# Optimization experiments

Measured on AMD Instinct MI355X. Metric: run time of the kernel, lower is better.

The kernel has to match this reference:

```python
import jax, jax.numpy as jnp
import numpy as np

N, E, F_IN, D, H = 20000, 640000, 128, 16, 8  # nodes, edges, in_features, out_features, n_heads


def _linear_params(k, fan_in, fan_out):
    W = jax.random.normal(k, (fan_in, fan_out), jnp.float32) / np.sqrt(fan_in)
    b = jnp.zeros((fan_out,), jnp.float32)
    return W, b


def setup_inputs() -> dict:
    key = jax.random.key(0)
    ks = jax.random.split(key, 8)
    x = jax.random.normal(ks[0], (N, F_IN), jnp.float32)
    edge_index = jax.random.randint(ks[1], (2, E), 0, N, dtype=jnp.int64)
    Wq, bq = _linear_params(ks[2], F_IN, D * H)
    Wk, bk = _linear_params(ks[3], F_IN, D * H)
    Wv, bv = _linear_params(ks[4], F_IN, D * H)
    Wpsi, bpsi = _linear_params(ks[5], D, D)
    Wo, bo = _linear_params(ks[6], D * H * 2, F_IN)
    gamma = jnp.ones((F_IN,), jnp.float32)
    beta = jnp.zeros((F_IN,), jnp.float32)
    return {"x": x, "edge_index": edge_index, "Wq": Wq, "bq": bq, "Wk": Wk, "bk": bk,
            "Wv": Wv, "bv": bv, "Wpsi": Wpsi, "bpsi": bpsi, "Wo": Wo, "bo": bo,
            "gamma": gamma, "beta": beta}


def _segment_softmax(logits, seg, num_segments):
    # numerically-stable softmax of edge logits grouped by destination node (row)
    m = jax.ops.segment_max(logits, seg, num_segments=num_segments)  # [N,H]
    m = jnp.where(jnp.isfinite(m), m, 0.0)
    e = jnp.exp(logits - m[seg])  # [E,H]
    s = jax.ops.segment_sum(e, seg, num_segments=num_segments)  # [N,H]
    return e / (s[seg] + 1e-16)


def reference(x, edge_index, Wq, bq, Wk, bk, Wv, bv, Wpsi, bpsi, Wo, bo, gamma, beta):
    q = (x @ Wq + bq).reshape(N, H, D)
    k = (x @ Wk + bk).reshape(N, H, D)
    v = (x @ Wv + bv).reshape(N, H, D)
    row, col = edge_index[0], edge_index[1]

    logits = jnp.einsum('ehd,ehd->eh', q[row], k[col]) / np.sqrt(D)  # [E,H]
    alpha = _segment_softmax(logits, row, N)  # [E,H]

    v_j = v[col]  # [E,H,D]
    h_lp = jax.ops.segment_sum((alpha[..., None] * v_j).reshape(E, H * D), row, num_segments=N)
    v_bp = jnp.tanh(v_j @ Wpsi + bpsi)  # per-head linear on last dim, [E,H,D]
    h_bp = jax.ops.segment_sum((alpha[..., None] * v_bp).reshape(E, H * D), row, num_segments=N)

    h_out = jnp.concatenate([h_lp, h_bp], axis=1) @ Wo + bo  # [N,F_IN]
    y = x + jax.nn.relu(h_out)
    mu = jnp.mean(y, axis=-1, keepdims=True)
    var = jnp.mean(jnp.square(y - mu), axis=-1, keepdims=True)
    return (y - mu) * jax.lax.rsqrt(var + 1e-5) * gamma + beta
```

## Files before the change

kernel.cpp:

```cpp
#include <hip/hip_runtime.h>
#include <hip/hip_bf16.h>
#include <math.h>

#define NN 20000
#define EE 640000

typedef __attribute__((ext_vector_type(8))) short short8;
typedef __attribute__((ext_vector_type(4))) float f32x4;
typedef __hip_bfloat16 bf16;

__device__ inline ushort f2bf(float f) {
  bf16 h = __float2bfloat16(f);
  return *(ushort*)&h;
}
__device__ inline float bflo(uint u) { return __uint_as_float(u << 16); }
__device__ inline float bfhi(uint u) { return __uint_as_float(u & 0xFFFF0000u); }

__global__ __launch_bounds__(256) void prep_scatter(
    const float* __restrict__ x, const int* __restrict__ ei,
    const float* __restrict__ Wq, const float* __restrict__ Wk,
    const float* __restrict__ Wv, const float* __restrict__ Wo,
    const float* __restrict__ Wpsi, const float* __restrict__ bpsi,
    const float* __restrict__ bv,
    ushort* __restrict__ xb, ushort* __restrict__ Wts,
    ushort* __restrict__ Wot, float* __restrict__ bvpsi,
    int* __restrict__ cursor, int* __restrict__ scol) {
  __shared__ float T[128][65];
  __shared__ float WpsiS[256];
  __shared__ float bpsiS[16];
  int b = blockIdx.x, t = threadIdx.x;

  if (b < 2500) {
    int e = b * 256 + t;
    int r = ei[e];
    int c = ei[EE + e];
    int pos = atomicAdd(&cursor[r], 1);
    if (pos < 128) scol[r * 128 + pos] = c;
    return;
  }
  if (b < 3750) {
    int idx = (b - 2500) * 2048 + t * 8;
    float4 f0 = *(const float4*)(x + idx);
    float4 f1 = *(const float4*)(x + idx + 4);
    ushort tmp[8] = {f2bf(f0.x), f2bf(f0.y), f2bf(f0.z), f2bf(f0.w),
                     f2bf(f1.x), f2bf(f1.y), f2bf(f1.z), f2bf(f1.w)};
    *(uint4*)(xb + idx) = *(uint4*)tmp;
    return;
  }
  if (b <= 3754) {
    int which = b - 3750;
    const float* W;
    int k0 = 0, dstride;
    ushort* dst;
    if (which < 3) { W = (which == 0) ? Wq : (which == 1 ? Wk : Wv);
                     dst = Wts + which * 16384; dstride = 128; }
    else { W = Wo; k0 = (which - 3) * 128; dst = Wot; dstride = 256; }
    for (int h2 = 0; h2 < 2; ++h2) {
      int r = t >> 1, c0 = (t & 1) * 32;
      const float* src = W + (size_t)(k0 + r) * 128 + h2 * 64 + c0;
#pragma unroll
      for (int j = 0; j < 8; ++j) {
        float4 f = *(const float4*)(src + 4 * j);
        T[r][c0 + 4 * j + 0] = f.x; T[r][c0 + 4 * j + 1] = f.y;
        T[r][c0 + 4 * j + 2] = f.z; T[r][c0 + 4 * j + 3] = f.w;
      }
      __syncthreads();
      int nl = t >> 2, kc = (t & 3) * 32;
      int n = h2 * 64 + nl;
      ushort buf[32];
#pragma unroll
      for (int k = 0; k < 32; ++k) buf[k] = f2bf(T[kc + k][nl]);
      ushort* dp = dst + (size_t)n * dstride + k0 + kc;
#pragma unroll
      for (int j = 0; j < 4; ++j) *(uint4*)(dp + 8 * j) = ((uint4*)buf)[j];
      __syncthreads();
    }
    return;
  }
  WpsiS[t] = Wpsi[t];
  if (t < 16) bpsiS[t] = bpsi[t];
  for (int h2 = 0; h2 < 2; ++h2) {
    int r = t >> 1, c0 = (t & 1) * 32;
    const float* src = Wv + (size_t)r * 128 + h2 * 64 + c0;
#pragma unroll
    for (int j = 0; j < 8; ++j) {
      float4 f = *(const float4*)(src + 4 * j);
      T[r][c0 + 4 * j + 0] = f.x; T[r][c0 + 4 * j + 1] = f.y;
      T[r][c0 + 4 * j + 2] = f.z; T[r][c0 + 4 * j + 3] = f.w;
    }
    __syncthreads();
    int nl = t >> 2, kc = (t & 3) * 32;
    int n = h2 * 64 + nl;
    int hh = n >> 4, dd = n & 15;
    int lcb = hh * 16 - h2 * 64;
    ushort buf[32];
    for (int k = 0; k < 32; ++k) {
      float acc = 0.f;
#pragma unroll
      for (int dp = 0; dp < 16; ++dp)
        acc = fmaf(T[kc + k][lcb + dp], WpsiS[dp * 16 + dd], acc);
      buf[k] = f2bf(acc);
    }
    ushort* dp2 = Wts + 3 * 16384 + (size_t)n * 128 + kc;
#pragma unroll
    for (int j = 0; j < 4; ++j) *(uint4*)(dp2 + 8 * j) = ((uint4*)buf)[j];
    __syncthreads();
  }
  if (t < 128) {
    int hh = t >> 4, dd = t & 15;
    float acc = bpsiS[dd];
#pragma unroll
    for (int dp = 0; dp < 16; ++dp)
      acc = fmaf(bv[hh * 16 + dp], WpsiS[dp * 16 + dd], acc);
    bvpsi[t] = acc;
  }
}

__global__ __launch_bounds__(256) void qkv_mfma(
    const ushort* __restrict__ xb, const ushort* __restrict__ Wts,
    const float* __restrict__ bq, const float* __restrict__ bk,
    const float* __restrict__ bv, const float* __restrict__ bvpsi,
    ushort* __restrict__ qb, ushort* __restrict__ kvb) {
  __shared__ ushort Tile[128 * 136];
  int t = threadIdx.x;
  int w = t >> 6, lane = t & 63;
  int m = lane & 15, qd = lane >> 4;
  int n0 = blockIdx.x * 128;
  int mat = blockIdx.y;
  const ushort* Wt = Wts + mat * 16384;
  const float* bias = (mat == 0) ? bq : (mat == 1 ? bk : (mat == 2 ? bv : bvpsi));
  int gr0 = n0 + w * 32;

  f32x4 acc0[8], acc1[8];
#pragma unroll
  for (int c = 0; c < 8; ++c) {
    acc0[c] = (f32x4){0.f, 0.f, 0.f, 0.f};
    acc1[c] = (f32x4){0.f, 0.f, 0.f, 0.f};
  }
#pragma unroll
  for (int kb = 0; kb < 4; ++kb) {
    int ko = kb * 32 + qd * 8;
    short8 a0 = *(const short8*)(xb + (size_t)(gr0 + m) * 128 + ko);
    short8 a1 = *(const short8*)(xb + (size_t)(gr0 + 16 + m) * 128 + ko);
#pragma unroll
    for (int c = 0; c < 8; ++c) {
      short8 bfr = *(const short8*)(Wt + (size_t)(c * 16 + m) * 128 + ko);
      acc0[c] = __builtin_amdgcn_mfma_f32_16x16x32_bf16(a0, bfr, acc0[c], 0, 0, 0);
      acc1[c] = __builtin_amdgcn_mfma_f32_16x16x32_bf16(a1, bfr, acc1[c], 0, 0, 0);
    }
  }
#pragma unroll
  for (int c = 0; c < 8; ++c) {
    int col = c * 16 + m;
    float bb = bias[col];
#pragma unroll
    for (int reg = 0; reg < 4; ++reg) {
      float v0 = acc0[c][reg] + bb;
      float v1 = acc1[c][reg] + bb;
      if (mat == 3) { v0 = tanhf(v0); v1 = tanhf(v1); }
      Tile[(w * 32 + 4 * qd + reg) * 136 + col] = f2bf(v0);
      Tile[(w * 32 + 16 + 4 * qd + reg) * 136 + col] = f2bf(v1);
    }
  }
  __syncthreads();
  int row = t >> 1, half = (t & 1) * 64;
  int grow = n0 + row;
  if (grow < NN) {
    const ushort* srcl = &Tile[row * 136 + half];
    ushort* dstg;
    if (mat == 0) dstg = qb + (size_t)grow * 128 + half;
    else dstg = kvb + (size_t)grow * 384 + (mat == 1 ? 0 : (mat == 2 ? 128 : 256)) + half;
#pragma unroll
    for (int j = 0; j < 8; ++j)
      *(uint4*)(dstg + 8 * j) = *(const uint4*)(srcl + 8 * j);
  }
}

__global__ __launch_bounds__(256) void aggregate_kernel(
    const ushort* __restrict__ qb, const ushort* __restrict__ kvb,
    const int* __restrict__ cursor, const int* __restrict__ scol,
    ushort* __restrict__ hb) {
  int wid = threadIdx.x >> 6, lane = threadIdx.x & 63;
  int node = blockIdx.x * 2 + (wid >> 1);
  int e = lane >> 2, h = (wid & 1) * 4 + (lane & 3);
  const float SC = 0.25f * 1.44269504f;

  float qv[16];
  {
    const ushort* qp = qb + (size_t)node * 128 + h * 16;
    uint4 a = *(const uint4*)qp;
    uint4 b = *(const uint4*)(qp + 8);
    uint qq[8] = {a.x, a.y, a.z, a.w, b.x, b.y, b.z, b.w};
#pragma unroll
    for (int i = 0; i < 8; ++i) {
      qv[2 * i] = bflo(qq[i]) * SC;
      qv[2 * i + 1] = bfhi(qq[i]) * SC;
    }
  }
  int cnt = cursor[node];
  cnt = cnt > 128 ? 128 : cnt;
  int base = node * 128;

  float s = 0.f;
  float accV[16], accB[16];
#pragma unroll
  for (int j = 0; j < 16; ++j) { accV[j] = 0.f; accB[j] = 0.f; }

  for (int i0 = 0; i0 < cnt; i0 += 16) {
    int idx = i0 + e;
    bool valid = idx < cnt;
    int col = scol[base + (valid ? idx : 0)];
    const ushort* B = kvb + (size_t)col * 384 + h * 16;
    uint4 ka = *(const uint4*)(B);
    uint4 kb4 = *(const uint4*)(B + 8);
    uint4 va = *(const uint4*)(B + 128);
    uint4 vb4 = *(const uint4*)(B + 136);
    uint4 ta = *(const uint4*)(B + 256);
    uint4 tb4 = *(const uint4*)(B + 264);
    uint kk[8] = {ka.x, ka.y, ka.z, ka.w, kb4.x, kb4.y, kb4.z, kb4.w};
    uint vv[8] = {va.x, va.y, va.z, va.w, vb4.x, vb4.y, vb4.z, vb4.w};
    uint tt[8] = {ta.x, ta.y, ta.z, ta.w, tb4.x, tb4.y, tb4.z, tb4.w};
    float d = 0.f;
#pragma unroll
    for (int i = 0; i < 8; ++i) {
      d = fmaf(qv[2 * i], bflo(kk[i]), d);
      d = fmaf(qv[2 * i + 1], bfhi(kk[i]), d);
    }
    float wgt = valid ? exp2f(d) : 0.f;
    s += wgt;
#pragma unroll
    for (int i = 0; i < 8; ++i) {
      accV[2 * i]     = fmaf(wgt, bflo(vv[i]), accV[2 * i]);
      accV[2 * i + 1] = fmaf(wgt, bfhi(vv[i]), accV[2 * i + 1]);
      accB[2 * i]     = fmaf(wgt, bflo(tt[i]), accB[2 * i]);
      accB[2 * i + 1] = fmaf(wgt, bfhi(tt[i]), accB[2 * i + 1]);
    }
  }

  s += __shfl_xor(s, 32);
#pragma unroll
  for (int j = 0; j < 16; ++j) {
    accV[j] += __shfl_xor(accV[j], 32);
    accB[j] += __shfl_xor(accB[j], 32);
  }
  bool pickV = e < 8;
  float sel[16];
#pragma unroll
  for (int j = 0; j < 16; ++j) sel[j] = pickV ? accV[j] : accB[j];
#pragma unroll
  for (int mask = 4; mask <= 16; mask <<= 1) {
    s += __shfl_xor(s, mask);
#pragma unroll
    for (int j = 0; j < 16; ++j) sel[j] += __shfl_xor(sel[j], mask);
  }
  float inv = s > 0.f ? 1.f / s : 0.f;
  int dg = pickV ? 2 * e : 2 * (e - 8);
  ushort* hp = hb + (size_t)node * 256 + (pickV ? 0 : 128) + h * 16 + dg;
  uint u = (uint)f2bf(sel[dg] * inv) | ((uint)f2bf(sel[dg + 1] * inv) << 16);
  *(uint*)hp = u;
}

__global__ __launch_bounds__(128) void output_mfma(
    const ushort* __restrict__ hb, const ushort* __restrict__ Wot,
    const float* __restrict__ x, const float* __restrict__ bo,
    const float* __restrict__ gamma, const float* __restrict__ beta,
    float* __restrict__ out) {
  int t = threadIdx.x;
  int w = t >> 6, lane = t & 63;
  int m = lane & 15, qd = lane >> 4;
  int gr0 = blockIdx.x * 64 + w * 32;

  f32x4 acc0[8], acc1[8];
#pragma unroll
  for (int c = 0; c < 8; ++c) {
    acc0[c] = (f32x4){0.f, 0.f, 0.f, 0.f};
    acc1[c] = (f32x4){0.f, 0.f, 0.f, 0.f};
  }
#pragma unroll
  for (int kb = 0; kb < 8; ++kb) {
    int ko = kb * 32 + qd * 8;
    short8 a0 = *(const short8*)(hb + (size_t)(gr0 + m) * 256 + ko);
    short8 a1 = *(const short8*)(hb + (size_t)(gr0 + 16 + m) * 256 + ko);
#pragma unroll
    for (int c = 0; c < 8; ++c) {
      short8 bfr = *(const short8*)(Wot + (size_t)(c * 16 + m) * 256 + ko);
      acc0[c] = __builtin_amdgcn_mfma_f32_16x16x32_bf16(a0, bfr, acc0[c], 0, 0, 0);
      acc1[c] = __builtin_amdgcn_mfma_f32_16x16x32_bf16(a1, bfr, acc1[c], 0, 0, 0);
    }
  }
#pragma unroll
  for (int half = 0; half < 2; ++half) {
#pragma unroll
    for (int reg = 0; reg < 4; ++reg) {
      int row = gr0 + half * 16 + 4 * qd + reg;
      bool valid = row < NN;
      float vals[8];
      float sum = 0.f;
#pragma unroll
      for (int c = 0; c < 8; ++c) {
        int col = c * 16 + m;
        float a = (half ? acc1[c][reg] : acc0[c][reg]) + bo[col];
        a = fmaxf(a, 0.f);
        float xv = valid ? x[(size_t)row * 128 + col] : 0.f;
        float v = a + xv;
        vals[c] = v;
        sum += v;
      }
      sum += __shfl_xor(sum, 1); sum += __shfl_xor(sum, 2);
      sum += __shfl_xor(sum, 4); sum += __shfl_xor(sum, 8);
      float mean = sum * (1.f / 128.f);
      float ssq = 0.f;
#pragma unroll
      for (int c = 0; c < 8; ++c) {
        float d = vals[c] - mean;
        ssq = fmaf(d, d, ssq);
      }
      ssq += __shfl_xor(ssq, 1); ssq += __shfl_xor(ssq, 2);
      ssq += __shfl_xor(ssq, 4); ssq += __shfl_xor(ssq, 8);
      float rstd = rsqrtf(ssq * (1.f / 128.f) + 1e-5f);
      if (valid) {
#pragma unroll
        for (int c = 0; c < 8; ++c) {
          int col = c * 16 + m;
          out[(size_t)row * 128 + col] =
              (vals[c] - mean) * rstd * gamma[col] + beta[col];
        }
      }
    }
  }
}

extern "C" void kernel_launch(void* const* d_in, const int* in_sizes, int n_in,
                              void* d_out, int out_size, void* d_ws, size_t ws_size,
                              hipStream_t stream) {
  const float* x     = (const float*)d_in[0];
  const int*   ei    = (const int*)d_in[1];
  const float* Wq    = (const float*)d_in[2];
  const float* bq    = (const float*)d_in[3];
  const float* Wk    = (const float*)d_in[4];
  const float* bk    = (const float*)d_in[5];
  const float* Wv    = (const float*)d_in[6];
  const float* bv    = (const float*)d_in[7];
  const float* Wpsi  = (const float*)d_in[8];
  const float* bpsi  = (const float*)d_in[9];
  const float* Wo    = (const float*)d_in[10];
  const float* bo    = (const float*)d_in[11];
  const float* gamma = (const float*)d_in[12];
  const float* beta  = (const float*)d_in[13];
  float* out = (float*)d_out;

  char* ws = (char*)d_ws;
  ushort* xb    = (ushort*)(ws);
  ushort* qb    = (ushort*)(ws + 5144576);
  ushort* Wts   = (ushort*)(ws + 10289152);
  ushort* Wot   = (ushort*)(ws + 10420224);
  float*  bvpsi = (float*) (ws + 10485760);
  ushort* kvb   = (ushort*)(ws + 10486272);
  ushort* hb    = (ushort*)(ws + 25846272);
  int*    cursor= (int*)   (ws + 36135424);
  int*    scol  = (int*)   (ws + 36215552);

  hipMemsetAsync(cursor, 0, 80000, stream);

  prep_scatter<<<3756, 256, 0, stream>>>(x, ei, Wq, Wk, Wv, Wo, Wpsi, bpsi, bv,
                                         xb, Wts, Wot, bvpsi, cursor, scol);
  qkv_mfma<<<dim3(157, 4), 256, 0, stream>>>(xb, Wts, bq, bk, bv, bvpsi, qb, kvb);
  aggregate_kernel<<<10000, 256, 0, stream>>>(qb, kvb, cursor, scol, hb);
  output_mfma<<<314, 128, 0, stream>>>(hb, Wot, x, bo, gamma, beta, out);
}
```

Before: 247.6 us.

## Pipeline edge gathers in aggregation, stage weights in LDS, coalesce output stores

The aggregation kernel now gives each wave one node, with 8 edges by 8 heads per wave instead of two waves per node. It preloads all neighbour column indices into registers and double-buffers the K/V/psi gathers so the next edge's loads overlap the current edge's arithmetic. Both MFMA GEMM kernels stage their weight matrix in shared memory rather than re-reading it from global memory. The output kernel also writes through an LDS tile to get coalesced float4 stores. These trade more registers and shared memory per block, which can lower occupancy, for better memory-level parallelism and fewer redundant global loads; the output grid also drops from 314 to 313 blocks.

```diff
diff --git a/kernel.cpp b/kernel.cpp
--- a/kernel.cpp
+++ b/kernel.cpp
@@ -121,14 +121,23 @@
     const float* __restrict__ bq, const float* __restrict__ bk,
     const float* __restrict__ bv, const float* __restrict__ bvpsi,
     ushort* __restrict__ qb, ushort* __restrict__ kvb) {
-  __shared__ ushort Tile[128 * 136];
+  __shared__ ushort Bs[128 * 136];
   int t = threadIdx.x;
-  int w = t >> 6, lane = t & 63;
-  int m = lane & 15, qd = lane >> 4;
   int n0 = blockIdx.x * 128;
   int mat = blockIdx.y;
   const ushort* Wt = Wts + mat * 16384;
   const float* bias = (mat == 0) ? bq : (mat == 1 ? bk : (mat == 2 ? bv : bvpsi));
+
+#pragma unroll
+  for (int j = 0; j < 8; ++j) {
+    int idx = j * 256 + t;
+    int row = idx >> 4, ko = (idx & 15) * 8;
+    *(uint4*)&Bs[row * 136 + ko] = *(const uint4*)(Wt + idx * 8);
+  }
+  __syncthreads();
+
+  int w = t >> 6, lane = t & 63;
+  int m = lane & 15, qd = lane >> 4;
   int gr0 = n0 + w * 32;
 
   f32x4 acc0[8], acc1[8];
@@ -144,11 +153,12 @@
     short8 a1 = *(const short8*)(xb + (size_t)(gr0 + 16 + m) * 128 + ko);
 #pragma unroll
     for (int c = 0; c < 8; ++c) {
-      short8 bfr = *(const short8*)(Wt + (size_t)(c * 16 + m) * 128 + ko);
+      short8 bfr = *(const short8*)&Bs[(c * 16 + m) * 136 + ko];
       acc0[c] = __builtin_amdgcn_mfma_f32_16x16x32_bf16(a0, bfr, acc0[c], 0, 0, 0);
       acc1[c] = __builtin_amdgcn_mfma_f32_16x16x32_bf16(a1, bfr, acc1[c], 0, 0, 0);
     }
   }
+  __syncthreads();
 #pragma unroll
   for (int c = 0; c < 8; ++c) {
     int col = c * 16 + m;
@@ -158,18 +168,18 @@
       float v0 = acc0[c][reg] + bb;
       float v1 = acc1[c][reg] + bb;
       if (mat == 3) { v0 = tanhf(v0); v1 = tanhf(v1); }
-      Tile[(w * 32 + 4 * qd + reg) * 136 + col] = f2bf(v0);
-      Tile[(w * 32 + 16 + 4 * qd + reg) * 136 + col] = f2bf(v1);
+      Bs[(w * 32 + 4 * qd + reg) * 136 + col] = f2bf(v0);
+      Bs[(w * 32 + 16 + 4 * qd + reg) * 136 + col] = f2bf(v1);
     }
   }
   __syncthreads();
   int row = t >> 1, half = (t & 1) * 64;
   int grow = n0 + row;
   if (grow < NN) {
-    const ushort* srcl = &Tile[row * 136 + half];
-    ushort* dstg;
-    if (mat == 0) dstg = qb + (size_t)grow * 128 + half;
-    else dstg = kvb + (size_t)grow * 384 + (mat == 1 ? 0 : (mat == 2 ? 128 : 256)) + half;
+    const ushort* srcl = &Bs[row * 136 + half];
+    ushort* dstg = (mat == 0)
+        ? qb + (size_t)grow * 128 + half
+        : kvb + (size_t)grow * 384 + (mat == 1 ? 0 : (mat == 2 ? 128 : 256)) + half;
 #pragma unroll
     for (int j = 0; j < 8; ++j)
       *(uint4*)(dstg + 8 * j) = *(const uint4*)(srcl + 8 * j);
@@ -181,8 +191,8 @@
     const int* __restrict__ cursor, const int* __restrict__ scol,
     ushort* __restrict__ hb) {
   int wid = threadIdx.x >> 6, lane = threadIdx.x & 63;
-  int node = blockIdx.x * 2 + (wid >> 1);
-  int e = lane >> 2, h = (wid & 1) * 4 + (lane & 3);
+  int node = blockIdx.x * 4 + wid;
+  int e = lane >> 3, h = lane & 7;
   const float SC = 0.25f * 1.44269504f;
 
   float qv[16];
@@ -200,33 +210,41 @@
   int cnt = cursor[node];
   cnt = cnt > 128 ? 128 : cnt;
   int base = node * 128;
+  int nv = (cnt + 7) >> 3;
+
+  int cols[16];
+#pragma unroll
+  for (int v = 0; v < 16; ++v) {
+    int idx = v * 8 + e;
+    cols[v] = scol[base + (idx < cnt ? idx : 0)];
+  }
 
   float s = 0.f;
   float accV[16], accB[16];
 #pragma unroll
   for (int j = 0; j < 16; ++j) { accV[j] = 0.f; accB[j] = 0.f; }
 
-  for (int i0 = 0; i0 < cnt; i0 += 16) {
-    int idx = i0 + e;
-    bool valid = idx < cnt;
-    int col = scol[base + (valid ? idx : 0)];
-    const ushort* B = kvb + (size_t)col * 384 + h * 16;
-    uint4 ka = *(const uint4*)(B);
-    uint4 kb4 = *(const uint4*)(B + 8);
-    uint4 va = *(const uint4*)(B + 128);
-    uint4 vb4 = *(const uint4*)(B + 136);
-    uint4 ta = *(const uint4*)(B + 256);
-    uint4 tb4 = *(const uint4*)(B + 264);
-    uint kk[8] = {ka.x, ka.y, ka.z, ka.w, kb4.x, kb4.y, kb4.z, kb4.w};
-    uint vv[8] = {va.x, va.y, va.z, va.w, vb4.x, vb4.y, vb4.z, vb4.w};
-    uint tt[8] = {ta.x, ta.y, ta.z, ta.w, tb4.x, tb4.y, tb4.z, tb4.w};
+  uint4 rA[6], rB[6];
+  auto FETCH = [&](int v, uint4* r) {
+    const ushort* B = kvb + (size_t)cols[v] * 384 + h * 16;
+    r[0] = *(const uint4*)(B);
+    r[1] = *(const uint4*)(B + 8);
+    r[2] = *(const uint4*)(B + 128);
+    r[3] = *(const uint4*)(B + 136);
+    r[4] = *(const uint4*)(B + 256);
+    r[5] = *(const uint4*)(B + 264);
+  };
+  auto CONSUME = [&](int v, const uint4* r) {
+    uint kk[8] = {r[0].x, r[0].y, r[0].z, r[0].w, r[1].x, r[1].y, r[1].z, r[1].w};
+    uint vv[8] = {r[2].x, r[2].y, r[2].z, r[2].w, r[3].x, r[3].y, r[3].z, r[3].w};
+    uint tt[8] = {r[4].x, r[4].y, r[4].z, r[4].w, r[5].x, r[5].y, r[5].z, r[5].w};
     float d = 0.f;
 #pragma unroll
     for (int i = 0; i < 8; ++i) {
       d = fmaf(qv[2 * i], bflo(kk[i]), d);
       d = fmaf(qv[2 * i + 1], bfhi(kk[i]), d);
     }
-    float wgt = valid ? exp2f(d) : 0.f;
+    float wgt = (v * 8 + e < cnt) ? exp2f(d) : 0.f;
     s += wgt;
 #pragma unroll
     for (int i = 0; i < 8; ++i) {
@@ -235,29 +253,35 @@
       accB[2 * i]     = fmaf(wgt, bflo(tt[i]), accB[2 * i]);
       accB[2 * i + 1] = fmaf(wgt, bfhi(tt[i]), accB[2 * i + 1]);
     }
-  }
-
-  s += __shfl_xor(s, 32);
-#pragma unroll
-  for (int j = 0; j < 16; ++j) {
-    accV[j] += __shfl_xor(accV[j], 32);
-    accB[j] += __shfl_xor(accB[j], 32);
-  }
-  bool pickV = e < 8;
-  float sel[16];
-#pragma unroll
-  for (int j = 0; j < 16; ++j) sel[j] = pickV ? accV[j] : accB[j];
-#pragma unroll
-  for (int mask = 4; mask <= 16; mask <<= 1) {
+  };
+
+  if (nv > 0) {
+    FETCH(0, rA);
+    int v = 0;
+    for (; v + 2 <= nv; v += 2) {
+      FETCH(v + 1, rB);
+      CONSUME(v, rA);
+      if (v + 2 < nv) FETCH(v + 2, rA);
+      CONSUME(v + 1, rB);
+    }
+    if (v < nv) CONSUME(v, rA);
+  }
+
+#pragma unroll
+  for (int mask = 8; mask <= 32; mask <<= 1) {
     s += __shfl_xor(s, mask);
 #pragma unroll
-    for (int j = 0; j < 16; ++j) sel[j] += __shfl_xor(sel[j], mask);
+    for (int j = 0; j < 16; ++j) {
+      accV[j] += __shfl_xor(accV[j], mask);
+      accB[j] += __shfl_xor(accB[j], mask);
+    }
   }
   float inv = s > 0.f ? 1.f / s : 0.f;
-  int dg = pickV ? 2 * e : 2 * (e - 8);
-  ushort* hp = hb + (size_t)node * 256 + (pickV ? 0 : 128) + h * 16 + dg;
-  uint u = (uint)f2bf(sel[dg] * inv) | ((uint)f2bf(sel[dg + 1] * inv) << 16);
-  *(uint*)hp = u;
+  int dg = 2 * e;
+  ushort* hp = hb + (size_t)node * 256 + h * 16 + dg;
+  *(uint*)hp = (uint)f2bf(accV[dg] * inv) | ((uint)f2bf(accV[dg + 1] * inv) << 16);
+  *(uint*)(hp + 128) =
+      (uint)f2bf(accB[dg] * inv) | ((uint)f2bf(accB[dg + 1] * inv) << 16);
 }
 
 __global__ __launch_bounds__(128) void output_mfma(
@@ -265,7 +289,16 @@
     const float* __restrict__ x, const float* __restrict__ bo,
     const float* __restrict__ gamma, const float* __restrict__ beta,
     float* __restrict__ out) {
+  __shared__ ushort Bs[128 * 264];
   int t = threadIdx.x;
+#pragma unroll
+  for (int j = 0; j < 32; ++j) {
+    int idx = j * 128 + t;
+    int row = idx >> 5, ko = (idx & 31) * 8;
+    *(uint4*)&Bs[row * 264 + ko] = *(const uint4*)(Wot + idx * 8);
+  }
+  __syncthreads();
+
   int w = t >> 6, lane = t & 63;
   int m = lane & 15, qd = lane >> 4;
   int gr0 = blockIdx.x * 64 + w * 32;
@@ -283,16 +316,19 @@
     short8 a1 = *(const short8*)(hb + (size_t)(gr0 + 16 + m) * 256 + ko);
 #pragma unroll
     for (int c = 0; c < 8; ++c) {
-      short8 bfr = *(const short8*)(Wot + (size_t)(c * 16 + m) * 256 + ko);
+      short8 bfr = *(const short8*)&Bs[(c * 16 + m) * 264 + ko];
       acc0[c] = __builtin_amdgcn_mfma_f32_16x16x32_bf16(a0, bfr, acc0[c], 0, 0, 0);
       acc1[c] = __builtin_amdgcn_mfma_f32_16x16x32_bf16(a1, bfr, acc1[c], 0, 0, 0);
     }
   }
+  __syncthreads();
+  float* Tile = (float*)Bs;
 #pragma unroll
   for (int half = 0; half < 2; ++half) {
 #pragma unroll
     for (int reg = 0; reg < 4; ++reg) {
-      int row = gr0 + half * 16 + 4 * qd + reg;
+      int lrow = w * 32 + half * 16 + 4 * qd + reg;
+      int row = blockIdx.x * 64 + lrow;
       bool valid = row < NN;
       float vals[8];
       float sum = 0.f;
@@ -318,15 +354,22 @@
       ssq += __shfl_xor(ssq, 1); ssq += __shfl_xor(ssq, 2);
       ssq += __shfl_xor(ssq, 4); ssq += __shfl_xor(ssq, 8);
       float rstd = rsqrtf(ssq * (1.f / 128.f) + 1e-5f);
-      if (valid) {
-#pragma unroll
-        for (int c = 0; c < 8; ++c) {
-          int col = c * 16 + m;
-          out[(size_t)row * 128 + col] =
-              (vals[c] - mean) * rstd * gamma[col] + beta[col];
-        }
+#pragma unroll
+      for (int c = 0; c < 8; ++c) {
+        int col = c * 16 + m;
+        Tile[lrow * 132 + col] = (vals[c] - mean) * rstd * gamma[col] + beta[col];
       }
     }
+  }
+  __syncthreads();
+  int row = t >> 1, cb = (t & 1) * 64;
+  int grow = blockIdx.x * 64 + row;
+  if (grow < NN) {
+    const float* srcl = &Tile[row * 132 + cb];
+    float* dstg = out + (size_t)grow * 128 + cb;
+#pragma unroll
+    for (int j = 0; j < 16; ++j)
+      *(float4*)(dstg + 4 * j) = *(const float4*)(srcl + 4 * j);
   }
 }
 
@@ -365,6 +408,6 @@
   prep_scatter<<<3756, 256, 0, stream>>>(x, ei, Wq, Wk, Wv, Wo, Wpsi, bpsi, bv,
                                          xb, Wts, Wot, bvpsi, cursor, scol);
   qkv_mfma<<<dim3(157, 4), 256, 0, stream>>>(xb, Wts, bq, bk, bv, bvpsi, qb, kvb);
-  aggregate_kernel<<<10000, 256, 0, stream>>>(qb, kvb, cursor, scol, hb);
-  output_mfma<<<314, 128, 0, stream>>>(hb, Wot, x, bo, gamma, beta, out);
-}
+  aggregate_kernel<<<5000, 256, 0, stream>>>(qb, kvb, cursor, scol, hb);
+  output_mfma<<<313, 128, 0, stream>>>(hb, Wot, x, bo, gamma, beta, out);
+}
```

Measured after the change: 242.3 us. 1.02x faster.
